# Performance work log

Measured on AMD Instinct MI355X. Metric: run time of the kernel, lower is better.

Reference implementation:

```python
import jax, jax.numpy as jnp
import numpy as np

B, N, DIM = 2, 4096, 512
HEADS, HEAD_DIM = 8, 64
INNER = HEADS * HEAD_DIM


def setup_inputs() -> dict:
    key = jax.random.key(0)
    k1, k2, k3 = jax.random.split(key, 3)
    x = jax.random.normal(k1, (B, N, DIM), dtype=jnp.float32)
    w_qkv = jax.random.normal(k2, (DIM, 3 * INNER), dtype=jnp.float32) * (DIM ** -0.5)
    temperature = jnp.asarray(np.log(HEAD_DIM ** -0.5), dtype=jnp.float32)
    w_out = jax.random.normal(k3, (INNER, DIM), dtype=jnp.float32) * (INNER ** -0.5)
    b_out = jnp.zeros((DIM,), dtype=jnp.float32)
    return {"x": x, "w_qkv": w_qkv, "temperature": temperature, "w_out": w_out, "b_out": b_out}


def reference(x, w_qkv, temperature, w_out, b_out):
    b, n, _ = x.shape
    qkv = x @ w_qkv                                   # (B, N, 3*inner)
    q, k, v = jnp.split(qkv, 3, axis=-1)
    # Faithful to original: raw reshape (NOT transpose) into (B, H, N, d)
    q = q.reshape(b, HEADS, n, HEAD_DIM)
    k = k.reshape(b, HEADS, n, HEAD_DIM)
    v = v.reshape(b, HEADS, n, HEAD_DIM)
    scores = jnp.einsum('bhnd,bhmd->bhnm', q, k) * jnp.exp(temperature)
    mask = jnp.eye(n, dtype=bool)                     # diagonal self-mask
    mask_value = jnp.finfo(scores.dtype).min
    scores = jnp.where(mask, mask_value, scores)
    attn = jax.nn.softmax(scores, axis=-1)
    out = jnp.einsum('bhnm,bhmd->bhnd', attn, v)      # (B, H, N, d)
    # Faithful to original: raw reshape (NOT transpose) back to (B, N, H*d)
    out = out.reshape(b, n, HEADS * HEAD_DIM)
    return out @ w_out + b_out                        # dropout inactive at inference
```

## Files before the change

### kernel.cpp

```cpp
#include <hip/hip_runtime.h>


typedef __bf16 bf16;
typedef __bf16 bf16x8 __attribute__((ext_vector_type(8)));
typedef __bf16 bf16x4 __attribute__((ext_vector_type(4)));
typedef __bf16 bf16x2 __attribute__((ext_vector_type(2)));
typedef float  f32x4  __attribute__((ext_vector_type(4)));
typedef float  f32x16 __attribute__((ext_vector_type(16)));
typedef unsigned u32x4 __attribute__((ext_vector_type(4)));

#define MFMA_BF16(a, b, c)   __builtin_amdgcn_mfma_f32_16x16x32_bf16((a), (b), (c), 0, 0, 0)
#define MFMA32_BF16(a, b, c) __builtin_amdgcn_mfma_f32_32x32x16_bf16((a), (b), (c), 0, 0, 0)

__device__ __forceinline__ void gld_lds16(void* lds, const void* g) {
  __builtin_amdgcn_global_load_lds(
      (const __attribute__((address_space(1))) void*)g,
      (__attribute__((address_space(3))) void*)lds, 16, 0, 0);
}

__device__ __forceinline__ unsigned pkbf(float a, float b) {
  bf16x2 t; t[0] = (bf16)a; t[1] = (bf16)b;
  return __builtin_bit_cast(unsigned, t);
}


__global__ void cast4_kernel(const float* __restrict__ in, bf16* __restrict__ out, int n4) {
  int i = blockIdx.x * 256 + threadIdx.x;
  if (i >= n4) return;
  float4 v = ((const float4*)in)[i];
  bf16x4 o;
  o[0] = (bf16)v.x; o[1] = (bf16)v.y; o[2] = (bf16)v.z; o[3] = (bf16)v.w;
  *(bf16x4*)(out + 4 * i) = o;
}

__global__ void wtrans_kernel(const float* __restrict__ in, bf16* __restrict__ out, int C) {
  __shared__ float tile[64 * 65];
  const int t = threadIdx.x;
  const int c0 = blockIdx.x * 64, r0 = blockIdx.y * 64;
#pragma unroll
  for (int p = 0; p < 16; p++) {
    int idx = p * 256 + t, r = idx >> 6, c = idx & 63;
    tile[r * 65 + c] = in[(r0 + r) * C + c0 + c];
  }
  __syncthreads();
#pragma unroll
  for (int p = 0; p < 16; p++) {
    int idx = p * 256 + t, c = idx >> 6, r = idx & 63;
    out[(size_t)(c0 + c) * 512 + r0 + r] = (bf16)tile[r * 65 + c];
  }
}

__global__ void vtrans_kernel(const bf16* __restrict__ V, bf16* __restrict__ Vt) {
  __shared__ bf16 tile[64 * 65];
  const int t = threadIdx.x;
  const size_t base = (size_t)blockIdx.y << 18;
  const int n0 = blockIdx.x * 64;
#pragma unroll
  for (int p = 0; p < 16; p++) {
    int idx = p * 256 + t, r = idx >> 6, c = idx & 63;
    tile[r * 65 + c] = V[base + (size_t)(n0 + r) * 64 + c];
  }
  __syncthreads();
#pragma unroll
  for (int p = 0; p < 16; p++) {
    int idx = p * 256 + t, d = idx >> 6, n = idx & 63;
    Vt[base + (size_t)d * 4096 + n0 + n] = tile[n * 65 + d];
  }
}


template<int EPI, int WNT>
__global__ __launch_bounds__(256) void gemm_bt(
    const bf16* __restrict__ A, const bf16* __restrict__ Bt,
    bf16* __restrict__ oQ, bf16* __restrict__ oK, bf16* __restrict__ oV,
    float* __restrict__ oC, const float* __restrict__ bias,
    const float* __restrict__ temp)
{
  __shared__ bf16 As[128 * 32];
  __shared__ bf16 Bs[WNT * 32 * 32];

  const int t    = threadIdx.x;
  const int lane = t & 63;
  const int w    = t >> 6;
  const int mm   = lane & 15;
  const int q    = lane >> 4;
  const int wm   = w >> 1, wn = w & 1;
  const int m0   = blockIdx.y * 128;
  const int n0   = blockIdx.x * (WNT * 32);

  const int srow = t >> 2, sch = t & 3;
  const int gch  = sch ^ ((srow >> 1) & 3);
  const bf16* Ab = A  + (m0 + srow) * 512 + gch * 8;
  const bf16* Bb = Bt + (n0 + srow) * 512 + gch * 8;
  bf16* Asl = As + t * 8;
  bf16* Bsl = Bs + t * 8;

  const int fslot = (q ^ ((mm >> 1) & 3)) * 8;

  const f32x4 zero4 = {0.f, 0.f, 0.f, 0.f};
  f32x4 acc[4][WNT];
#pragma unroll
  for (int i = 0; i < 4; i++)
#pragma unroll
    for (int j = 0; j < WNT; j++) acc[i][j] = zero4;

  for (int k0 = 0; k0 < 512; k0 += 32) {
    __syncthreads();
    gld_lds16(Asl,        Ab + k0);
    gld_lds16(Asl + 2048, Ab + 64 * 512 + k0);
    gld_lds16(Bsl,        Bb + k0);
    if (WNT == 4) gld_lds16(Bsl + 2048, Bb + 64 * 512 + k0);
    __syncthreads();

    bf16x8 af[4], bfv[WNT];
#pragma unroll
    for (int i = 0; i < 4; i++)
      af[i] = *(const bf16x8*)(As + (wm * 64 + i * 16 + mm) * 32 + fslot);
#pragma unroll
    for (int j = 0; j < WNT; j++)
      bfv[j] = *(const bf16x8*)(Bs + (wn * (WNT * 16) + j * 16 + mm) * 32 + fslot);

#pragma unroll
    for (int i = 0; i < 4; i++)
#pragma unroll
      for (int j = 0; j < WNT; j++)
        acc[i][j] = MFMA_BF16(af[i], bfv[j], acc[i][j]);
  }

  if (EPI == 0) {
    const float scale = __expf(temp[0]) * 1.44269504088896f;
#pragma unroll
    for (int i = 0; i < 4; i++) {
      const int row = m0 + wm * 64 + i * 16 + q * 4;
#pragma unroll
      for (int j = 0; j < WNT; j++) {
        const int col = n0 + wn * (WNT * 16) + j * 16 + mm;
        bf16* dst; int c2; float s;
        if (col < 512)       { dst = oQ; c2 = col;        s = scale; }
        else if (col < 1024) { dst = oK; c2 = col - 512;  s = 1.0f;  }
        else                 { dst = oV; c2 = col - 1024; s = 1.0f;  }
#pragma unroll
        for (int r = 0; r < 4; r++)
          dst[(size_t)(row + r) * 512 + c2] = (bf16)(acc[i][j][r] * s);
      }
    }
  } else {
#pragma unroll
    for (int i = 0; i < 4; i++) {
      const int row = m0 + wm * 64 + i * 16 + q * 4;
#pragma unroll
      for (int j = 0; j < WNT; j++) {
        const int col = n0 + wn * (WNT * 16) + j * 16 + mm;
        const float b = bias[col];
#pragma unroll
        for (int r = 0; r < 4; r++)
          oC[(size_t)(row + r) * 512 + col] = acc[i][j][r] + b;
      }
    }
  }
}


template<int SPLIT>
__global__ __launch_bounds__(256, 2) void attn_kernel(
    const bf16* __restrict__ Q, const bf16* __restrict__ Kb,
    const bf16* __restrict__ Vt, bf16* __restrict__ O,
    float* __restrict__ Opart, float* __restrict__ Lpart)
{
  __shared__ bf16 Ks[2][64 * 64];
  __shared__ bf16 Vs[2][64 * 64];
  __shared__ float rsum[4][64];

  const int t    = threadIdx.x;
  const int lane = t & 63;
  const int w    = t >> 6;
  const int c32  = lane & 31;
  const int h    = lane >> 5;
  const int pxa  = (lane ^ 32) << 2;
  const int bh   = blockIdx.y;
  const int q0   = blockIdx.x * 256;
  const int z    = blockIdx.z;
  const size_t hb = (size_t)bh << 18;
  const bf16* Qh = Q  + hb;
  const bf16* Kh = Kb + hb;
  const bf16* Vh = Vt + hb;
  const int q0w  = q0 + w * 64;

  int tlo, tn;
  if (SPLIT == 1)      { tlo = 0;                               tn = 64; }
  else if (SPLIT == 2) { tlo = z * 32;                          tn = 32; }
  else                 { tlo = (z == 0) ? 0 : (z == 1 ? 22 : 43); tn = (z == 0) ? 22 : 21; }

  bf16x8 qf[2][4];
#pragma unroll
  for (int qt = 0; qt < 2; qt++)
#pragma unroll
    for (int s = 0; s < 4; s++)
      qf[qt][s] = *(const bf16x8*)(Qh + (size_t)(q0w + qt * 32 + c32) * 64 + s * 16 + h * 8);

  f32x16 o[2][2];
#pragma unroll
  for (int qt = 0; qt < 2; qt++)
#pragma unroll
    for (int dt = 0; dt < 2; dt++)
#pragma unroll
      for (int r = 0; r < 16; r++) o[qt][dt][r] = 0.f;
  float lacc[2] = {0.f, 0.f};

  const int r0 = t >> 3, c0 = t & 7;
  const int g0 = c0 ^ (r0 & 7);
  const bf16* Kg = Kh + (size_t)r0 * 64 + g0 * 8;
  const bf16* Vg = Vh + (size_t)r0 * 4096 + g0 * 8;

  {
    const int kv0 = tlo * 64;
    gld_lds16(&Ks[0][t * 8],        Kg + (size_t)kv0 * 64);
    gld_lds16(&Ks[0][t * 8] + 2048, Kg + (size_t)(kv0 + 32) * 64);
    gld_lds16(&Vs[0][t * 8],        Vg + kv0);
    gld_lds16(&Vs[0][t * 8] + 2048, Vg + (size_t)32 * 4096 + kv0);
  }

  for (int it = 0; it < tn; it++) {
    const int cur = it & 1;
    if (it + 1 < tn) {
      const int kv1 = (tlo + it + 1) * 64;
      bf16* Kn = &Ks[cur ^ 1][t * 8];
      bf16* Vn = &Vs[cur ^ 1][t * 8];
      gld_lds16(Kn,        Kg + (size_t)kv1 * 64);
      gld_lds16(Kn + 2048, Kg + (size_t)(kv1 + 32) * 64);
      gld_lds16(Vn,        Vg + kv1);
      gld_lds16(Vn + 2048, Vg + (size_t)32 * 4096 + kv1);
      __asm__ volatile("s_waitcnt vmcnt(4)" ::: "memory");
    } else {
      __asm__ volatile("s_waitcnt vmcnt(0)" ::: "memory");
    }
    __builtin_amdgcn_s_barrier();
    __asm__ volatile("" ::: "memory");

    const int kv0 = (tlo + it) * 64;
    const bool diag = (kv0 == q0w);
    const bf16* Kc = Ks[cur];
    const bf16* Vc = Vs[cur];

#pragma unroll
    for (int kt = 0; kt < 2; kt++) {
      bf16x8 kf[4];
      const int kr = kt * 32 + c32;
#pragma unroll
      for (int s = 0; s < 4; s++)
        kf[s] = *(const bf16x8*)(Kc + kr * 64 + (((s << 1) | h) ^ (kr & 7)) * 8);

      bf16x8 pa[2][2];
#pragma unroll
      for (int qt = 0; qt < 2; qt++) {
        f32x16 sv;
#pragma unroll
        for (int r = 0; r < 16; r++) sv[r] = 0.f;
        __builtin_amdgcn_s_setprio(1);
#pragma unroll
        for (int s = 0; s < 4; s++)
          sv = MFMA32_BF16(kf[s], qf[qt][s], sv);
        __builtin_amdgcn_s_setprio(0);

        float pp[16];
#pragma unroll
        for (int r = 0; r < 16; r++) pp[r] = __builtin_amdgcn_exp2f(sv[r]);
        if (diag && kt == qt) {
#pragma unroll
          for (int r = 0; r < 16; r++)
            if (c32 == ((r & 3) + ((r >> 2) << 3) + (h << 2))) pp[r] = 0.f;
        }
        float s8[8];
#pragma unroll
        for (int r = 0; r < 8; r++) s8[r] = pp[r] + pp[r + 8];
        float s4[4];
#pragma unroll
        for (int r = 0; r < 4; r++) s4[r] = s8[r] + s8[r + 4];
        lacc[qt] += (s4[0] + s4[1]) + (s4[2] + s4[3]);

#pragma unroll
        for (int s2 = 0; s2 < 2; s2++) {
          const int b = s2 * 8;
          unsigned wa = pkbf(pp[b + 0], pp[b + 1]);
          unsigned wc = pkbf(pp[b + 2], pp[b + 3]);
          unsigned wb = pkbf(pp[b + 4], pp[b + 5]);
          unsigned wd = pkbf(pp[b + 6], pp[b + 7]);
          unsigned r1 = (unsigned)__builtin_amdgcn_ds_bpermute(pxa, (int)(h ? wa : wb));
          unsigned r2 = (unsigned)__builtin_amdgcn_ds_bpermute(pxa, (int)(h ? wc : wd));
          u32x4 wv;
          wv[0] = h ? r1 : wa;
          wv[1] = h ? r2 : wc;
          wv[2] = h ? wb : r1;
          wv[3] = h ? wd : r2;
          pa[qt][s2] = __builtin_bit_cast(bf16x8, wv);
        }
      }

#pragma unroll
      for (int s2 = 0; s2 < 2; s2++) {
        bf16x8 vf[2];
#pragma unroll
        for (int dt = 0; dt < 2; dt++) {
          const int d = dt * 32 + c32;
          vf[dt] = *(const bf16x8*)(Vc + d * 64 + (((((kt << 1) | s2) << 1) | h) ^ (d & 7)) * 8);
        }
        __builtin_amdgcn_s_setprio(1);
#pragma unroll
        for (int qt = 0; qt < 2; qt++)
#pragma unroll
          for (int dt = 0; dt < 2; dt++)
            o[qt][dt] = MFMA32_BF16(pa[qt][s2], vf[dt], o[qt][dt]);
        __builtin_amdgcn_s_setprio(0);
      }
    }
    __asm__ volatile("" ::: "memory");
    __builtin_amdgcn_s_barrier();
  }

  float tot[2];
#pragma unroll
  for (int qt = 0; qt < 2; qt++) {
    const int pb = __builtin_amdgcn_ds_bpermute(pxa, __builtin_bit_cast(int, lacc[qt]));
    tot[qt] = lacc[qt] + __builtin_bit_cast(float, pb);
  }

  if (SPLIT == 1) {
    bf16* Oh = O + hb;
#pragma unroll
    for (int qt = 0; qt < 2; qt++)
      if (h == 0) rsum[w][qt * 32 + c32] = tot[qt];
    __asm__ volatile("s_waitcnt lgkmcnt(0)" ::: "memory");
#pragma unroll
    for (int qt = 0; qt < 2; qt++) {
#pragma unroll
      for (int r = 0; r < 16; r++) {
        const int row = (r & 3) + ((r >> 2) << 3) + (h << 2);
        const float rinv = 1.0f / rsum[w][qt * 32 + row];
#pragma unroll
        for (int dt = 0; dt < 2; dt++)
          Oh[(size_t)(q0w + qt * 32 + row) * 64 + dt * 32 + c32] =
              (bf16)(o[qt][dt][r] * rinv);
      }
    }
  } else {
    float* Op = Opart + ((size_t)z << 22) + hb;
    float* Lp = Lpart + (z << 16) + (bh << 12);
#pragma unroll
    for (int qt = 0; qt < 2; qt++) {
      if (h == 0) Lp[q0w + qt * 32 + c32] = tot[qt];
#pragma unroll
      for (int r = 0; r < 16; r++) {
        const int row = (r & 3) + ((r >> 2) << 3) + (h << 2);
#pragma unroll
        for (int dt = 0; dt < 2; dt++)
          Op[(size_t)(q0w + qt * 32 + row) * 64 + dt * 32 + c32] = o[qt][dt][r];
      }
    }
  }
}

template<int SPLIT>
__global__ void merge_kernel(const float* __restrict__ Op, const float* __restrict__ Lp,
                             bf16* __restrict__ Ob) {
  const int g = blockIdx.x * 256 + threadIdx.x;
  const int f = g * 4;
  const int row = f >> 6;
  float l = 0.f;
  float4 a = {0.f, 0.f, 0.f, 0.f};
#pragma unroll
  for (int zz = 0; zz < SPLIT; zz++) {
    l += Lp[(zz << 16) + row];
    const float4 b = *(const float4*)(Op + ((size_t)zz << 22) + f);
    a.x += b.x; a.y += b.y; a.z += b.z; a.w += b.w;
  }
  const float rinv = 1.0f / l;
  bf16x4 o;
  o[0] = (bf16)(a.x * rinv);
  o[1] = (bf16)(a.y * rinv);
  o[2] = (bf16)(a.z * rinv);
  o[3] = (bf16)(a.w * rinv);
  *(bf16x4*)(Ob + f) = o;
}


extern "C" void kernel_launch(void* const* d_in, const int* in_sizes, int n_in,
                              void* d_out, int out_size, void* d_ws, size_t ws_size,
                              hipStream_t stream) {
  const float* x      = (const float*)d_in[0];
  const float* w_qkv  = (const float*)d_in[1];
  const float* temp   = (const float*)d_in[2];
  const float* w_out  = (const float*)d_in[3];
  const float* b_out  = (const float*)d_in[4];
  float* out          = (float*)d_out;

  char* ws = (char*)d_ws;
  bf16*  Xb    = (bf16*)(ws);
  bf16*  Wt    = (bf16*)(ws + (size_t)(8u  << 20));
  bf16*  Qb    = (bf16*)(ws + (size_t)(10u << 20));
  bf16*  Kb    = (bf16*)(ws + (size_t)(18u << 20));
  bf16*  Vb    = (bf16*)(ws + (size_t)(26u << 20));
  bf16*  Vtb   = (bf16*)(ws + (size_t)(34u << 20));
  bf16*  Ob    = (bf16*)(ws + (size_t)(42u << 20));
  bf16*  Wot   = (bf16*)(ws + (size_t)(50u << 20));
  float* Lpart = (float*)(ws + (size_t)(51u << 20));
  float* Opart = (float*)(ws + (size_t)(52u << 20));

  const int split = (ws_size >= ((size_t)86u << 20)) ? 2 : 1;

  cast4_kernel<<<4096, 256, 0, stream>>>(x, Xb, (8192 * 512) / 4);
  wtrans_kernel<<<dim3(24, 8), 256, 0, stream>>>(w_qkv, Wt, 1536);
  wtrans_kernel<<<dim3(8, 8), 256, 0, stream>>>(w_out, Wot, 512);

  gemm_bt<0, 4><<<dim3(12, 64), 256, 0, stream>>>(Xb, Wt, Qb, Kb, Vb, nullptr, nullptr, temp);

  vtrans_kernel<<<dim3(64, 16), 256, 0, stream>>>(Vb, Vtb);

  if (split == 2) {
    attn_kernel<2><<<dim3(16, 16, 2), 256, 0, stream>>>(Qb, Kb, Vtb, nullptr, Opart, Lpart);
    merge_kernel<2><<<4096, 256, 0, stream>>>(Opart, Lpart, Ob);
  } else {
    attn_kernel<1><<<dim3(16, 16, 1), 256, 0, stream>>>(Qb, Kb, Vtb, Ob, nullptr, nullptr);
  }

  gemm_bt<1, 2><<<dim3(8, 64), 256, 0, stream>>>(Ob, Wot, nullptr, nullptr, nullptr, out, b_out, nullptr);
}
```

Measured before the change: 210.4 us.

## Halve attention query tile per block to 128 rows, raise occupancy to four blocks

Each wave of the attention kernel now handles 32 query rows instead of 64, so a block covers 128 queries and the grid doubles along the query axis. Launch bounds move from 2 to 4 blocks per CU, since the smaller register footprint allows more waves to hide latency. In exchange, every K/V tile loaded into LDS is reused by half as many queries, which doubles global K/V traffic and the number of barriers per unit of work. The diagonal mask test is adjusted to match the new 32-row wave offsets.

```diff
diff --git a/kernel.cpp b/kernel.cpp
--- a/kernel.cpp
+++ b/kernel.cpp
@@ -162,14 +162,14 @@
 
 
 template<int SPLIT>
-__global__ __launch_bounds__(256, 2) void attn_kernel(
+__global__ __launch_bounds__(256, 4) void attn_kernel(
     const bf16* __restrict__ Q, const bf16* __restrict__ Kb,
     const bf16* __restrict__ Vt, bf16* __restrict__ O,
     float* __restrict__ Opart, float* __restrict__ Lpart)
 {
   __shared__ bf16 Ks[2][64 * 64];
   __shared__ bf16 Vs[2][64 * 64];
-  __shared__ float rsum[4][64];
+  __shared__ float rsum[4][32];
 
   const int t    = threadIdx.x;
   const int lane = t & 63;
@@ -178,39 +178,37 @@
   const int h    = lane >> 5;
   const int pxa  = (lane ^ 32) << 2;
   const int bh   = blockIdx.y;
-  const int q0   = blockIdx.x * 256;
+  const int q0   = blockIdx.x * 128;
   const int z    = blockIdx.z;
   const size_t hb = (size_t)bh << 18;
   const bf16* Qh = Q  + hb;
   const bf16* Kh = Kb + hb;
   const bf16* Vh = Vt + hb;
-  const int q0w  = q0 + w * 64;
+  const int q0w  = q0 + w * 32;
 
   int tlo, tn;
-  if (SPLIT == 1)      { tlo = 0;                               tn = 64; }
-  else if (SPLIT == 2) { tlo = z * 32;                          tn = 32; }
-  else                 { tlo = (z == 0) ? 0 : (z == 1 ? 22 : 43); tn = (z == 0) ? 22 : 21; }
-
-  bf16x8 qf[2][4];
-#pragma unroll
-  for (int qt = 0; qt < 2; qt++)
-#pragma unroll
-    for (int s = 0; s < 4; s++)
-      qf[qt][s] = *(const bf16x8*)(Qh + (size_t)(q0w + qt * 32 + c32) * 64 + s * 16 + h * 8);
-
-  f32x16 o[2][2];
-#pragma unroll
-  for (int qt = 0; qt < 2; qt++)
-#pragma unroll
-    for (int dt = 0; dt < 2; dt++)
-#pragma unroll
-      for (int r = 0; r < 16; r++) o[qt][dt][r] = 0.f;
-  float lacc[2] = {0.f, 0.f};
+  if (SPLIT == 1)      { tlo = 0;      tn = 64; }
+  else                 { tlo = z * 32; tn = 32; }
+
+  bf16x8 qf[4];
+#pragma unroll
+  for (int s = 0; s < 4; s++)
+    qf[s] = *(const bf16x8*)(Qh + (size_t)(q0w + c32) * 64 + s * 16 + h * 8);
+
+  f32x16 o[2];
+#pragma unroll
+  for (int dt = 0; dt < 2; dt++)
+#pragma unroll
+    for (int r = 0; r < 16; r++) o[dt][r] = 0.f;
+  float lacc = 0.f;
 
   const int r0 = t >> 3, c0 = t & 7;
   const int g0 = c0 ^ (r0 & 7);
   const bf16* Kg = Kh + (size_t)r0 * 64 + g0 * 8;
   const bf16* Vg = Vh + (size_t)r0 * 4096 + g0 * 8;
+
+  const int dbase = q0w & ~63;
+  const int kthalf = (q0w >> 5) & 1;
 
   {
     const int kv0 = tlo * 64;
@@ -238,7 +236,7 @@
     __asm__ volatile("" ::: "memory");
 
     const int kv0 = (tlo + it) * 64;
-    const bool diag = (kv0 == q0w);
+    const bool diag = (kv0 == dbase);
     const bf16* Kc = Ks[cur];
     const bf16* Vc = Vs[cur];
 
@@ -250,50 +248,47 @@
       for (int s = 0; s < 4; s++)
         kf[s] = *(const bf16x8*)(Kc + kr * 64 + (((s << 1) | h) ^ (kr & 7)) * 8);
 
-      bf16x8 pa[2][2];
-#pragma unroll
-      for (int qt = 0; qt < 2; qt++) {
-        f32x16 sv;
-#pragma unroll
-        for (int r = 0; r < 16; r++) sv[r] = 0.f;
-        __builtin_amdgcn_s_setprio(1);
-#pragma unroll
-        for (int s = 0; s < 4; s++)
-          sv = MFMA32_BF16(kf[s], qf[qt][s], sv);
-        __builtin_amdgcn_s_setprio(0);
-
-        float pp[16];
-#pragma unroll
-        for (int r = 0; r < 16; r++) pp[r] = __builtin_amdgcn_exp2f(sv[r]);
-        if (diag && kt == qt) {
-#pragma unroll
-          for (int r = 0; r < 16; r++)
-            if (c32 == ((r & 3) + ((r >> 2) << 3) + (h << 2))) pp[r] = 0.f;
-        }
-        float s8[8];
-#pragma unroll
-        for (int r = 0; r < 8; r++) s8[r] = pp[r] + pp[r + 8];
-        float s4[4];
-#pragma unroll
-        for (int r = 0; r < 4; r++) s4[r] = s8[r] + s8[r + 4];
-        lacc[qt] += (s4[0] + s4[1]) + (s4[2] + s4[3]);
-
-#pragma unroll
-        for (int s2 = 0; s2 < 2; s2++) {
-          const int b = s2 * 8;
-          unsigned wa = pkbf(pp[b + 0], pp[b + 1]);
-          unsigned wc = pkbf(pp[b + 2], pp[b + 3]);
-          unsigned wb = pkbf(pp[b + 4], pp[b + 5]);
-          unsigned wd = pkbf(pp[b + 6], pp[b + 7]);
-          unsigned r1 = (unsigned)__builtin_amdgcn_ds_bpermute(pxa, (int)(h ? wa : wb));
-          unsigned r2 = (unsigned)__builtin_amdgcn_ds_bpermute(pxa, (int)(h ? wc : wd));
-          u32x4 wv;
-          wv[0] = h ? r1 : wa;
-          wv[1] = h ? r2 : wc;
-          wv[2] = h ? wb : r1;
-          wv[3] = h ? wd : r2;
-          pa[qt][s2] = __builtin_bit_cast(bf16x8, wv);
-        }
+      f32x16 sv;
+#pragma unroll
+      for (int r = 0; r < 16; r++) sv[r] = 0.f;
+      __builtin_amdgcn_s_setprio(1);
+#pragma unroll
+      for (int s = 0; s < 4; s++)
+        sv = MFMA32_BF16(kf[s], qf[s], sv);
+      __builtin_amdgcn_s_setprio(0);
+
+      float pp[16];
+#pragma unroll
+      for (int r = 0; r < 16; r++) pp[r] = __builtin_amdgcn_exp2f(sv[r]);
+      if (diag && kt == kthalf) {
+#pragma unroll
+        for (int r = 0; r < 16; r++)
+          if (c32 == ((r & 3) + ((r >> 2) << 3) + (h << 2))) pp[r] = 0.f;
+      }
+      float s8[8];
+#pragma unroll
+      for (int r = 0; r < 8; r++) s8[r] = pp[r] + pp[r + 8];
+      float s4[4];
+#pragma unroll
+      for (int r = 0; r < 4; r++) s4[r] = s8[r] + s8[r + 4];
+      lacc += (s4[0] + s4[1]) + (s4[2] + s4[3]);
+
+      bf16x8 pa[2];
+#pragma unroll
+      for (int s2 = 0; s2 < 2; s2++) {
+        const int b = s2 * 8;
+        unsigned wa = pkbf(pp[b + 0], pp[b + 1]);
+        unsigned wc = pkbf(pp[b + 2], pp[b + 3]);
+        unsigned wb = pkbf(pp[b + 4], pp[b + 5]);
+        unsigned wd = pkbf(pp[b + 6], pp[b + 7]);
+        unsigned r1 = (unsigned)__builtin_amdgcn_ds_bpermute(pxa, (int)(h ? wa : wb));
+        unsigned r2 = (unsigned)__builtin_amdgcn_ds_bpermute(pxa, (int)(h ? wc : wd));
+        u32x4 wv;
+        wv[0] = h ? r1 : wa;
+        wv[1] = h ? r2 : wc;
+        wv[2] = h ? wb : r1;
+        wv[3] = h ? wd : r2;
+        pa[s2] = __builtin_bit_cast(bf16x8, wv);
       }
 
 #pragma unroll
@@ -306,10 +301,8 @@
         }
         __builtin_amdgcn_s_setprio(1);
 #pragma unroll
-        for (int qt = 0; qt < 2; qt++)
-#pragma unroll
-          for (int dt = 0; dt < 2; dt++)
-            o[qt][dt] = MFMA32_BF16(pa[qt][s2], vf[dt], o[qt][dt]);
+        for (int dt = 0; dt < 2; dt++)
+          o[dt] = MFMA32_BF16(pa[s2], vf[dt], o[dt]);
         __builtin_amdgcn_s_setprio(0);
       }
     }
@@ -317,44 +310,31 @@
     __builtin_amdgcn_s_barrier();
   }
 
-  float tot[2];
-#pragma unroll
-  for (int qt = 0; qt < 2; qt++) {
-    const int pb = __builtin_amdgcn_ds_bpermute(pxa, __builtin_bit_cast(int, lacc[qt]));
-    tot[qt] = lacc[qt] + __builtin_bit_cast(float, pb);
-  }
+  const int pb = __builtin_amdgcn_ds_bpermute(pxa, __builtin_bit_cast(int, lacc));
+  const float tot = lacc + __builtin_bit_cast(float, pb);
 
   if (SPLIT == 1) {
     bf16* Oh = O + hb;
-#pragma unroll
-    for (int qt = 0; qt < 2; qt++)
-      if (h == 0) rsum[w][qt * 32 + c32] = tot[qt];
+    if (h == 0) rsum[w][c32] = tot;
     __asm__ volatile("s_waitcnt lgkmcnt(0)" ::: "memory");
 #pragma unroll
-    for (int qt = 0; qt < 2; qt++) {
-#pragma unroll
-      for (int r = 0; r < 16; r++) {
-        const int row = (r & 3) + ((r >> 2) << 3) + (h << 2);
-        const float rinv = 1.0f / rsum[w][qt * 32 + row];
-#pragma unroll
-        for (int dt = 0; dt < 2; dt++)
-          Oh[(size_t)(q0w + qt * 32 + row) * 64 + dt * 32 + c32] =
-              (bf16)(o[qt][dt][r] * rinv);
-      }
+    for (int r = 0; r < 16; r++) {
+      const int row = (r & 3) + ((r >> 2) << 3) + (h << 2);
+      const float rinv = 1.0f / rsum[w][row];
+#pragma unroll
+      for (int dt = 0; dt < 2; dt++)
+        Oh[(size_t)(q0w + row) * 64 + dt * 32 + c32] = (bf16)(o[dt][r] * rinv);
     }
   } else {
     float* Op = Opart + ((size_t)z << 22) + hb;
     float* Lp = Lpart + (z << 16) + (bh << 12);
-#pragma unroll
-    for (int qt = 0; qt < 2; qt++) {
-      if (h == 0) Lp[q0w + qt * 32 + c32] = tot[qt];
-#pragma unroll
-      for (int r = 0; r < 16; r++) {
-        const int row = (r & 3) + ((r >> 2) << 3) + (h << 2);
-#pragma unroll
-        for (int dt = 0; dt < 2; dt++)
-          Op[(size_t)(q0w + qt * 32 + row) * 64 + dt * 32 + c32] = o[qt][dt][r];
-      }
+    if (h == 0) Lp[q0w + c32] = tot;
+#pragma unroll
+    for (int r = 0; r < 16; r++) {
+      const int row = (r & 3) + ((r >> 2) << 3) + (h << 2);
+#pragma unroll
+      for (int dt = 0; dt < 2; dt++)
+        Op[(size_t)(q0w + row) * 64 + dt * 32 + c32] = o[dt][r];
     }
   }
 }
@@ -416,10 +396,10 @@
   vtrans_kernel<<<dim3(64, 16), 256, 0, stream>>>(Vb, Vtb);
 
   if (split == 2) {
-    attn_kernel<2><<<dim3(16, 16, 2), 256, 0, stream>>>(Qb, Kb, Vtb, nullptr, Opart, Lpart);
+    attn_kernel<2><<<dim3(32, 16, 2), 256, 0, stream>>>(Qb, Kb, Vtb, nullptr, Opart, Lpart);
     merge_kernel<2><<<4096, 256, 0, stream>>>(Opart, Lpart, Ob);
   } else {
-    attn_kernel<1><<<dim3(16, 16, 1), 256, 0, stream>>>(Qb, Kb, Vtb, Ob, nullptr, nullptr);
+    attn_kernel<1><<<dim3(32, 16, 1), 256, 0, stream>>>(Qb, Kb, Vtb, Ob, nullptr, nullptr);
   }
 
   gemm_bt<1, 2><<<dim3(8, 64), 256, 0, stream>>>(Ob, Wot, nullptr, nullptr, nullptr, out, b_out, nullptr);
```

New measurement: 211.5 us. No clear change (+0.5%).
